# Performance work log

Hardware: AMD Instinct MI355X
Metric: run time of the kernel (lower is better)

Reference implementation:

```python
import jax, jax.numpy as jnp
import numpy as np

VOCAB = 50257
D_MODEL = 1024
PAD_IDX = 0
B, L = 4, 4096


def setup_inputs() -> dict:
    key = jax.random.key(0)
    k_emb, k_R, k_ids, k_role = jax.random.split(key, 4)
    emb = jax.random.normal(k_emb, (VOCAB, D_MODEL), dtype=jnp.float32)
    emb = emb.at[PAD_IDX].set(0.0)  # nn.Embedding padding_idx row is zero
    R = jax.random.normal(k_R, (D_MODEL, D_MODEL), dtype=jnp.float32)
    input_ids = jax.random.randint(k_ids, (B, L), 0, VOCAB, dtype=jnp.int64)
    role_mask = jax.random.randint(k_role, (B, L), 0, 2, dtype=jnp.int64)
    return {"input_ids": input_ids, "role_mask": role_mask, "emb": emb, "R": R}


def reference(input_ids, role_mask, emb, R):
    # embedding gather: (B, L, D)
    x = emb[input_ids]
    # agent tokens get x @ R.T, user tokens pass through
    agent = (role_mask == 1)[..., None]
    transformed = jnp.einsum('bld,ed->ble', x, R)
    return jnp.where(agent, transformed, x)
```

## Files before the change

### kernel.cpp

```cpp
#include <hip/hip_runtime.h>
#include <hip/hip_bf16.h>
#include <stdint.h>

#define DMODEL 1024
#define M_TOK  16384

typedef __attribute__((ext_vector_type(8))) short short8;
typedef __attribute__((ext_vector_type(4))) float f32x4;

__device__ __forceinline__ unsigned int pack2_bf16(float f0, float f1) {
    unsigned int u0 = __builtin_bit_cast(unsigned int, f0);
    unsigned int u1 = __builtin_bit_cast(unsigned int, f1);
    u0 += 0x7fffu + ((u0 >> 16) & 1u);
    u1 += 0x7fffu + ((u1 >> 16) & 1u);
    return __builtin_amdgcn_perm(u1, u0, 0x07060302);
}

__device__ __forceinline__ void gload_lds16(const void* g, void* l) {
    __builtin_amdgcn_global_load_lds(
        (const __attribute__((address_space(1))) void*)g,
        (__attribute__((address_space(3))) void*)l, 16, 0, 0);
}

__global__ void plan_compact(const int* __restrict__ roles,
                             int* __restrict__ pos, int* __restrict__ orig,
                             int* __restrict__ n_agent) {
    __shared__ int s[1024];
    const int t = threadIdx.x;
    int pred[16];
    int c = 0;
#pragma unroll
    for (int i = 0; i < 16; ++i) {
        pred[i] = (roles[i * 1024 + t] == 1);
        c += pred[i];
    }
    s[t] = c;
    __syncthreads();
    for (int off = 1; off < 1024; off <<= 1) {
        int v = (t >= off) ? s[t - off] : 0;
        __syncthreads();
        s[t] += v;
        __syncthreads();
    }
    int base = s[t] - c;
#pragma unroll
    for (int i = 0; i < 16; ++i) {
        if (pred[i]) {
            const int m = i * 1024 + t;
            orig[base] = m;
            pos[m] = base;
            ++base;
        }
    }
    if (t == 1023) *n_agent = s[1023];
}

__global__ void gather2(const int* __restrict__ ids, const int* __restrict__ roles,
                        const int* __restrict__ pos,
                        const float* __restrict__ emb, const float* __restrict__ Rm,
                        __hip_bfloat16* __restrict__ Xc,
                        __hip_bfloat16* __restrict__ Rb,
                        float* __restrict__ out) {
    const int row  = blockIdx.x * 4 + (threadIdx.x >> 6);
    const int lane = threadIdx.x & 63;
    if (row < M_TOK) {
        const float* src = emb + (size_t)ids[row] * DMODEL;
        if (roles[row] == 1) {
            __hip_bfloat16* dst = Xc + (size_t)pos[row] * DMODEL;
#pragma unroll
            for (int c = 0; c < 4; ++c) {
                const int idx = c * 256 + lane * 4;
                float4 v = *(const float4*)(src + idx);
                uint2 p = make_uint2(pack2_bf16(v.x, v.y), pack2_bf16(v.z, v.w));
                *(uint2*)((unsigned short*)dst + idx) = p;
            }
        } else {
            float* dst = out + (size_t)row * DMODEL;
#pragma unroll
            for (int c = 0; c < 4; ++c) {
                const int idx = c * 256 + lane * 4;
                *(float4*)(dst + idx) = *(const float4*)(src + idx);
            }
        }
    } else {
        const int r = row - M_TOK;
        const float* src = Rm + (size_t)r * DMODEL;
        __hip_bfloat16* dst = Rb + (size_t)r * DMODEL;
#pragma unroll
        for (int c = 0; c < 4; ++c) {
            const int idx = c * 256 + lane * 4;
            float4 v = *(const float4*)(src + idx);
            uint2 p = make_uint2(pack2_bf16(v.x, v.y), pack2_bf16(v.z, v.w));
            *(uint2*)((unsigned short*)dst + idx) = p;
        }
    }
}

__global__ void rse_gemm3(const int* __restrict__ n_agent_p,
                          const int* __restrict__ orig,
                          const __hip_bfloat16* __restrict__ Xc,
                          const __hip_bfloat16* __restrict__ Rb,
                          float* __restrict__ out) {
    const int na = *n_agent_p;
    const int m0 = blockIdx.x * 128;
    if (m0 >= na) return;
    const int n0 = blockIdx.y * 128;

    __shared__ __hip_bfloat16 As[128 * 32];
    __shared__ __hip_bfloat16 Bs[128 * 32];
    __shared__ int s_orig[128];

    const int tid  = threadIdx.x;
    const int lane = tid & 63;
    const int wave = tid >> 6;
    const int quad = lane >> 4;
    const int l15  = lane & 15;
    const int wr   = wave >> 1;
    const int wc   = wave & 1;

    if (tid < 128) {
        const int j = m0 + tid;
        s_orig[tid] = (j < na) ? orig[j] : -1;
    }

    const int st_row = lane >> 2;
    const int st_k   = (lane & 3) * 8;
    const int rg0 = wave * 16;
    const int rg1 = (4 + wave) * 16;

    const __hip_bfloat16* aG = Xc + (size_t)m0 * DMODEL;
    const __hip_bfloat16* bG = Rb + (size_t)n0 * DMODEL;

    f32x4 acc[4][4] = {};

    for (int k0 = 0; k0 < DMODEL; k0 += 32) {
        __syncthreads();
        gload_lds16(aG + (size_t)(rg0 + st_row) * DMODEL + k0 + st_k, &As[rg0 * 32]);
        gload_lds16(aG + (size_t)(rg1 + st_row) * DMODEL + k0 + st_k, &As[rg1 * 32]);
        gload_lds16(bG + (size_t)(rg0 + st_row) * DMODEL + k0 + st_k, &Bs[rg0 * 32]);
        gload_lds16(bG + (size_t)(rg1 + st_row) * DMODEL + k0 + st_k, &Bs[rg1 * 32]);
        __syncthreads();

        short8 af[4], bfr[4];
#pragma unroll
        for (int i = 0; i < 4; ++i)
            af[i] = *(const short8*)&As[(wr * 64 + i * 16 + l15) * 32 + quad * 8];
#pragma unroll
        for (int j = 0; j < 4; ++j)
            bfr[j] = *(const short8*)&Bs[(wc * 64 + j * 16 + l15) * 32 + quad * 8];
#pragma unroll
        for (int i = 0; i < 4; ++i)
#pragma unroll
            for (int j = 0; j < 4; ++j)
                acc[i][j] = __builtin_amdgcn_mfma_f32_16x16x32_bf16(af[i], bfr[j], acc[i][j], 0, 0, 0);
    }

    const int colbase = n0 + wc * 64 + l15;
#pragma unroll
    for (int ti = 0; ti < 4; ++ti) {
        const int rowb = wr * 64 + ti * 16 + quad * 4;
#pragma unroll
        for (int r = 0; r < 4; ++r) {
            const int row = rowb + r;
            const int oj  = s_orig[row];
            if (oj >= 0) {
                float* dst = out + (size_t)oj * DMODEL + colbase;
#pragma unroll
                for (int tj = 0; tj < 4; ++tj)
                    dst[tj * 16] = acc[ti][tj][r];
            }
        }
    }
}

extern "C" void kernel_launch(void* const* d_in, const int* in_sizes, int n_in,
                              void* d_out, int out_size, void* d_ws, size_t ws_size,
                              hipStream_t stream) {
    const int*   ids   = (const int*)d_in[0];
    const int*   roles = (const int*)d_in[1];
    const float* emb   = (const float*)d_in[2];
    const float* Rm    = (const float*)d_in[3];
    float*       out   = (float*)d_out;

    __hip_bfloat16* Xc = (__hip_bfloat16*)d_ws;
    __hip_bfloat16* Rb = Xc + (size_t)M_TOK * DMODEL;
    int* orig    = (int*)(Rb + (size_t)DMODEL * DMODEL);
    int* pos     = orig + M_TOK;
    int* n_agent = pos + M_TOK;

    plan_compact<<<1, 1024, 0, stream>>>(roles, pos, orig, n_agent);
    gather2<<<(M_TOK + DMODEL) / 4, 256, 0, stream>>>(ids, roles, pos, emb, Rm, Xc, Rb, out);
    dim3 grid2(M_TOK / 128, DMODEL / 128);
    rse_gemm3<<<grid2, 256, 0, stream>>>(n_agent, orig, Xc, Rb, out);
}
```

Before: 317.8 us.

## Fuse compaction into gather via atomics; widen GEMM K-tile with XOR-swizzled LDS

Replaces the single-block prefix-scan compaction kernel with per-block atomic slot allocation inside the gather kernel, which removes a serial launch and the pos array. The GEMM's K tile grows from 32 to 64 and the LDS layout gets an XOR swizzle, halving the number of barriers per K step and reducing bank conflicts. Compacted row order now depends on atomic ordering, which is harmless because orig maps each row back to its output position. A tiny zeroing kernel is added to reset the counter.

```diff
diff --git a/kernel.cpp b/kernel.cpp
--- a/kernel.cpp
+++ b/kernel.cpp
@@ -22,57 +22,45 @@
         (__attribute__((address_space(3))) void*)l, 16, 0, 0);
 }
 
-__global__ void plan_compact(const int* __restrict__ roles,
-                             int* __restrict__ pos, int* __restrict__ orig,
-                             int* __restrict__ n_agent) {
-    __shared__ int s[1024];
-    const int t = threadIdx.x;
-    int pred[16];
-    int c = 0;
+__global__ void zero_ctr(int* __restrict__ n_agent) { *n_agent = 0; }
+
+__global__ void __launch_bounds__(1024)
+gather3(const int* __restrict__ ids, const int* __restrict__ roles,
+        const float* __restrict__ emb, const float* __restrict__ Rm,
+        __hip_bfloat16* __restrict__ Xc, __hip_bfloat16* __restrict__ Rb,
+        float* __restrict__ out, int* __restrict__ orig,
+        int* __restrict__ n_agent) {
+    __shared__ int s_cnt[16];
+    __shared__ int s_slot[16];
+    const int wave = threadIdx.x >> 6;
+    const int lane = threadIdx.x & 63;
+    const int blk  = blockIdx.x;
+    if (blk < M_TOK / 16) {
+        const int row  = blk * 16 + wave;
+        const int id   = ids[row];
+        const int role = roles[row];
+        if (lane == 0) s_cnt[wave] = (role == 1);
+        __syncthreads();
+        if (threadIdx.x == 0) {
+            int tot = 0, pre[16];
 #pragma unroll
-    for (int i = 0; i < 16; ++i) {
-        pred[i] = (roles[i * 1024 + t] == 1);
-        c += pred[i];
-    }
-    s[t] = c;
-    __syncthreads();
-    for (int off = 1; off < 1024; off <<= 1) {
-        int v = (t >= off) ? s[t - off] : 0;
+            for (int w = 0; w < 16; ++w) { pre[w] = tot; tot += s_cnt[w]; }
+            const int base = atomicAdd(n_agent, tot);
+#pragma unroll
+            for (int w = 0; w < 16; ++w) s_slot[w] = base + pre[w];
+        }
         __syncthreads();
-        s[t] += v;
-        __syncthreads();
-    }
-    int base = s[t] - c;
-#pragma unroll
-    for (int i = 0; i < 16; ++i) {
-        if (pred[i]) {
-            const int m = i * 1024 + t;
-            orig[base] = m;
-            pos[m] = base;
-            ++base;
-        }
-    }
-    if (t == 1023) *n_agent = s[1023];
-}
-
-__global__ void gather2(const int* __restrict__ ids, const int* __restrict__ roles,
-                        const int* __restrict__ pos,
-                        const float* __restrict__ emb, const float* __restrict__ Rm,
-                        __hip_bfloat16* __restrict__ Xc,
-                        __hip_bfloat16* __restrict__ Rb,
-                        float* __restrict__ out) {
-    const int row  = blockIdx.x * 4 + (threadIdx.x >> 6);
-    const int lane = threadIdx.x & 63;
-    if (row < M_TOK) {
-        const float* src = emb + (size_t)ids[row] * DMODEL;
-        if (roles[row] == 1) {
-            __hip_bfloat16* dst = Xc + (size_t)pos[row] * DMODEL;
+        const float* src = emb + (size_t)id * DMODEL;
+        if (role == 1) {
+            const int slot = s_slot[wave];
+            if (lane == 0) orig[slot] = row;
+            unsigned short* dst = (unsigned short*)(Xc + (size_t)slot * DMODEL);
 #pragma unroll
             for (int c = 0; c < 4; ++c) {
                 const int idx = c * 256 + lane * 4;
                 float4 v = *(const float4*)(src + idx);
                 uint2 p = make_uint2(pack2_bf16(v.x, v.y), pack2_bf16(v.z, v.w));
-                *(uint2*)((unsigned short*)dst + idx) = p;
+                *(uint2*)(dst + idx) = p;
             }
         } else {
             float* dst = out + (size_t)row * DMODEL;
@@ -83,31 +71,31 @@
             }
         }
     } else {
-        const int r = row - M_TOK;
+        const int r = (blk - M_TOK / 16) * 16 + wave;
         const float* src = Rm + (size_t)r * DMODEL;
-        __hip_bfloat16* dst = Rb + (size_t)r * DMODEL;
+        unsigned short* dst = (unsigned short*)(Rb + (size_t)r * DMODEL);
 #pragma unroll
         for (int c = 0; c < 4; ++c) {
             const int idx = c * 256 + lane * 4;
             float4 v = *(const float4*)(src + idx);
             uint2 p = make_uint2(pack2_bf16(v.x, v.y), pack2_bf16(v.z, v.w));
-            *(uint2*)((unsigned short*)dst + idx) = p;
+            *(uint2*)(dst + idx) = p;
         }
     }
 }
 
-__global__ void rse_gemm3(const int* __restrict__ n_agent_p,
-                          const int* __restrict__ orig,
-                          const __hip_bfloat16* __restrict__ Xc,
-                          const __hip_bfloat16* __restrict__ Rb,
-                          float* __restrict__ out) {
+__global__ void __launch_bounds__(256)
+rse_gemm4(const int* __restrict__ n_agent_p, const int* __restrict__ orig,
+          const __hip_bfloat16* __restrict__ Xc,
+          const __hip_bfloat16* __restrict__ Rb,
+          float* __restrict__ out) {
     const int na = *n_agent_p;
     const int m0 = blockIdx.x * 128;
     if (m0 >= na) return;
     const int n0 = blockIdx.y * 128;
 
-    __shared__ __hip_bfloat16 As[128 * 32];
-    __shared__ __hip_bfloat16 Bs[128 * 32];
+    __shared__ __hip_bfloat16 As[128 * 64];
+    __shared__ __hip_bfloat16 Bs[128 * 64];
     __shared__ int s_orig[128];
 
     const int tid  = threadIdx.x;
@@ -123,36 +111,42 @@
         s_orig[tid] = (j < na) ? orig[j] : -1;
     }
 
-    const int st_row = lane >> 2;
-    const int st_k   = (lane & 3) * 8;
-    const int rg0 = wave * 16;
-    const int rg1 = (4 + wave) * 16;
-
-    const __hip_bfloat16* aG = Xc + (size_t)m0 * DMODEL;
-    const __hip_bfloat16* bG = Rb + (size_t)n0 * DMODEL;
+    const int st_row = lane >> 3;
+    const int st_k   = ((lane & 7) ^ st_row) * 8;
+    const __hip_bfloat16* aG = Xc + (size_t)m0 * DMODEL + st_k;
+    const __hip_bfloat16* bG = Rb + (size_t)n0 * DMODEL + st_k;
 
     f32x4 acc[4][4] = {};
 
-    for (int k0 = 0; k0 < DMODEL; k0 += 32) {
+    for (int k0 = 0; k0 < DMODEL; k0 += 64) {
         __syncthreads();
-        gload_lds16(aG + (size_t)(rg0 + st_row) * DMODEL + k0 + st_k, &As[rg0 * 32]);
-        gload_lds16(aG + (size_t)(rg1 + st_row) * DMODEL + k0 + st_k, &As[rg1 * 32]);
-        gload_lds16(bG + (size_t)(rg0 + st_row) * DMODEL + k0 + st_k, &Bs[rg0 * 32]);
-        gload_lds16(bG + (size_t)(rg1 + st_row) * DMODEL + k0 + st_k, &Bs[rg1 * 32]);
+#pragma unroll
+        for (int q = 0; q < 4; ++q) {
+            const int rg = (q * 4 + wave) * 8;
+            gload_lds16(aG + (size_t)(rg + st_row) * DMODEL + k0, &As[rg * 64]);
+            gload_lds16(bG + (size_t)(rg + st_row) * DMODEL + k0, &Bs[rg * 64]);
+        }
         __syncthreads();
 
-        short8 af[4], bfr[4];
 #pragma unroll
-        for (int i = 0; i < 4; ++i)
-            af[i] = *(const short8*)&As[(wr * 64 + i * 16 + l15) * 32 + quad * 8];
+        for (int kk = 0; kk < 2; ++kk) {
+            short8 af[4], bfr[4];
 #pragma unroll
-        for (int j = 0; j < 4; ++j)
-            bfr[j] = *(const short8*)&Bs[(wc * 64 + j * 16 + l15) * 32 + quad * 8];
+            for (int i = 0; i < 4; ++i) {
+                const int r = wr * 64 + i * 16 + l15;
+                af[i] = *(const short8*)&As[r * 64 + ((kk * 4 + quad) ^ (r & 7)) * 8];
+            }
 #pragma unroll
-        for (int i = 0; i < 4; ++i)
+            for (int j = 0; j < 4; ++j) {
+                const int r = wc * 64 + j * 16 + l15;
+                bfr[j] = *(const short8*)&Bs[r * 64 + ((kk * 4 + quad) ^ (r & 7)) * 8];
+            }
 #pragma unroll
-            for (int j = 0; j < 4; ++j)
-                acc[i][j] = __builtin_amdgcn_mfma_f32_16x16x32_bf16(af[i], bfr[j], acc[i][j], 0, 0, 0);
+            for (int i = 0; i < 4; ++i)
+#pragma unroll
+                for (int j = 0; j < 4; ++j)
+                    acc[i][j] = __builtin_amdgcn_mfma_f32_16x16x32_bf16(af[i], bfr[j], acc[i][j], 0, 0, 0);
+        }
     }
 
     const int colbase = n0 + wc * 64 + l15;
@@ -161,8 +155,7 @@
         const int rowb = wr * 64 + ti * 16 + quad * 4;
 #pragma unroll
         for (int r = 0; r < 4; ++r) {
-            const int row = rowb + r;
-            const int oj  = s_orig[row];
+            const int oj = s_orig[rowb + r];
             if (oj >= 0) {
                 float* dst = out + (size_t)oj * DMODEL + colbase;
 #pragma unroll
@@ -185,11 +178,11 @@
     __hip_bfloat16* Xc = (__hip_bfloat16*)d_ws;
     __hip_bfloat16* Rb = Xc + (size_t)M_TOK * DMODEL;
     int* orig    = (int*)(Rb + (size_t)DMODEL * DMODEL);
-    int* pos     = orig + M_TOK;
-    int* n_agent = pos + M_TOK;
+    int* n_agent = orig + M_TOK;
 
-    plan_compact<<<1, 1024, 0, stream>>>(roles, pos, orig, n_agent);
-    gather2<<<(M_TOK + DMODEL) / 4, 256, 0, stream>>>(ids, roles, pos, emb, Rm, Xc, Rb, out);
+    zero_ctr<<<1, 1, 0, stream>>>(n_agent);
+    gather3<<<M_TOK / 16 + DMODEL / 16, 1024, 0, stream>>>(
+        ids, roles, emb, Rm, Xc, Rb, out, orig, n_agent);
     dim3 grid2(M_TOK / 128, DMODEL / 128);
-    rse_gemm3<<<grid2, 256, 0, stream>>>(n_agent, orig, Xc, Rb, out);
+    rse_gemm4<<<grid2, 256, 0, stream>>>(n_agent, orig, Xc, Rb, out);
 }
```

New measurement: 309.8 us, median of 2. 1.03x faster.
